# Optimization experiments

Measured on AMD Instinct MI355X. Metric: run time of the kernel, lower is better.

## Reference

```python
import jax, jax.numpy as jnp
import numpy as np

S_LEN = 4096; HID = 2048
NH = 8; NVH = 16; DK = 128; DV = 128
KEY_DIM = NH * DK; VAL_DIM = NVH * DV
CONV = 4; EPS = 1e-6; GVA = NVH // NH
SCALE = DK ** -0.5


def _short_conv_silu(x, w):
    # causal depthwise conv1d + SiLU: x [S, C], w [C, K]
    K = w.shape[1]
    xp = jnp.pad(x, ((K - 1, 0), (0, 0)))
    y = xp[0:S_LEN] * w[:, 0]
    for j in range(1, K):
        y = y + xp[j:j + S_LEN] * w[:, j]
    return jax.nn.silu(y)


def _l2norm(x):
    return x / jnp.sqrt(jnp.sum(x * x, axis=-1, keepdims=True) + EPS)


def _forward(x, Wq, Wk, Wv, Wa, Wb, Wg, Wo, conv_q, conv_k, conv_v, A_log, dt_bias, w_norm):
    q = _short_conv_silu(x @ Wq.T, conv_q)   # [S, KEY_DIM]
    k = _short_conv_silu(x @ Wk.T, conv_k)
    v = _short_conv_silu(x @ Wv.T, conv_v)   # [S, VAL_DIM]
    q = q.reshape(S_LEN, NH, DK)
    k = k.reshape(S_LEN, NH, DK)
    v = v.reshape(S_LEN, NVH, DV)
    # grouped value attention: each k/q head serves GVA value heads
    q = jnp.repeat(q, GVA, axis=1)           # [S, NVH, DK]
    k = jnp.repeat(k, GVA, axis=1)
    q = _l2norm(q) * SCALE
    k = _l2norm(k)
    beta = jax.nn.sigmoid(x @ Wb.T)          # [S, NVH] delta-rule learning rate
    g = -jnp.exp(A_log) * jax.nn.softplus(x @ Wa.T + dt_bias)  # [S, NVH] log-decay <= 0

    def step(S, inp):
        q_t, k_t, v_t, g_t, b_t = inp        # [H,DK],[H,DK],[H,DV],[H],[H]
        S = S * jnp.exp(g_t)[:, None, None]  # gated decay of memory
        pred = jnp.einsum('hk,hkv->hv', k_t, S)
        delta = (v_t - pred) * b_t[:, None]  # delta-rule update direction
        S = S + jnp.einsum('hk,hv->hkv', k_t, delta)
        o_t = jnp.einsum('hk,hkv->hv', q_t, S)
        return S, o_t

    S0 = jnp.zeros((NVH, DK, DV), x.dtype)
    _, o = jax.lax.scan(step, S0, (q, k, v, g, beta))  # o [S, NVH, DV]

    # FusedRMSNormGated: gate with silu, then RMS-normalize over head_v_dim
    gate = (x @ Wg.T).reshape(S_LEN, NVH, DV)
    og = o * jax.nn.silu(gate)
    og = og * jax.lax.rsqrt(jnp.mean(og * og, axis=-1, keepdims=True) + EPS) * w_norm
    return og.reshape(S_LEN, VAL_DIM) @ Wo.T  # [S, HID]


def setup_inputs() -> dict:
    key = jax.random.key(0)
    ks = jax.random.split(key, 16)
    def lin(k, out_dim, in_dim):
        return jax.random.normal(k, (out_dim, in_dim), jnp.float32) * (in_dim ** -0.5)
    dt = jnp.exp(jax.random.uniform(ks[12], (NVH,)) * (np.log(0.1) - np.log(0.001)) + np.log(0.001))
    dt = jnp.maximum(dt, 1e-4)
    return {
        "x": jax.random.normal(ks[0], (S_LEN, HID), jnp.float32),
        "Wq": lin(ks[1], KEY_DIM, HID),
        "Wk": lin(ks[2], KEY_DIM, HID),
        "Wv": lin(ks[3], VAL_DIM, HID),
        "Wa": lin(ks[4], NVH, HID),
        "Wb": lin(ks[5], NVH, HID),
        "Wg": lin(ks[6], VAL_DIM, HID),
        "Wo": lin(ks[7], HID, VAL_DIM),
        "conv_q": jax.random.normal(ks[8], (KEY_DIM, CONV), jnp.float32) * 0.2,
        "conv_k": jax.random.normal(ks[9], (KEY_DIM, CONV), jnp.float32) * 0.2,
        "conv_v": jax.random.normal(ks[10], (VAL_DIM, CONV), jnp.float32) * 0.2,
        "A_log": jnp.log(jax.random.uniform(ks[11], (NVH,), minval=1.0, maxval=16.0)),
        "dt_bias": dt + jnp.log(-jnp.expm1(-dt)),
        "w_norm": jnp.ones((DV,), jnp.float32),
    }


def reference(x, Wq, Wk, Wv, Wa, Wb, Wg, Wo, conv_q, conv_k, conv_v, A_log, dt_bias, w_norm):
    return _forward(x, Wq, Wk, Wv, Wa, Wb, Wg, Wo, conv_q, conv_k, conv_v, A_log, dt_bias, w_norm)
```

## Files before the change

### kernel.cpp

```cpp
#include <hip/hip_runtime.h>
#include <hip/hip_bf16.h>
#include <math.h>

#define S_LEN 4096
#define HID   2048
#define NH    8
#define NVH   16
#define DK    128
#define DV    128
#define KEY_DIM  (NH*DK)
#define VAL_DIM  (NVH*DV)
#define SCALE_Q  0.08838834764831845f
#define CCH 64
#define NCH (S_LEN/CCH)

typedef __attribute__((ext_vector_type(8))) short short8;
typedef __attribute__((ext_vector_type(4))) float f32x4;

__global__ __launch_bounds__(256) void cast_f2b(
    const float* __restrict__ in, __hip_bfloat16* __restrict__ out, int n) {
  int i = (blockIdx.x * 256 + threadIdx.x) * 4;
  if (i >= n) return;
  float4 v = *(const float4*)&in[i];
  union { __hip_bfloat16 b[4]; short4 s; } u;
  u.b[0] = __float2bfloat16(v.x); u.b[1] = __float2bfloat16(v.y);
  u.b[2] = __float2bfloat16(v.z); u.b[3] = __float2bfloat16(v.w);
  *(short4*)&out[i] = u.s;
}

__device__ __forceinline__ void lds_load16(const __hip_bfloat16* g,
                                           __hip_bfloat16* l) {
  __builtin_amdgcn_global_load_lds(
      (const __attribute__((address_space(1))) unsigned int*)g,
      (__attribute__((address_space(3))) unsigned int*)l, 16, 0, 0);
}

__global__ __launch_bounds__(256) void gemm_bf16_bt(
    const __hip_bfloat16* __restrict__ A, const __hip_bfloat16* __restrict__ B,
    float* __restrict__ C, int M, int N, int K) {
  __shared__ __hip_bfloat16 sA[128 * 32];
  __shared__ __hip_bfloat16 sB[128 * 32];
  const int t = threadIdx.x;
  const int wave = t >> 6, lane = t & 63;
  const int bm = blockIdx.y, bn = blockIdx.x;
  const int wm = (wave & 1) * 64, wn = (wave >> 1) * 64;

  f32x4 zero = {0.f, 0.f, 0.f, 0.f};
  f32x4 acc[4][4];
  #pragma unroll
  for (int i = 0; i < 4; i++)
    #pragma unroll
    for (int j = 0; j < 4; j++) acc[i][j] = zero;

  const int r0 = t >> 2,        c0 = (t & 3) * 8;
  const int r1 = (256 + t) >> 2, c1 = ((256 + t) & 3) * 8;
  const __hip_bfloat16* gA0 = A + (size_t)(bm * 128 + r0) * K + c0;
  const __hip_bfloat16* gA1 = A + (size_t)(bm * 128 + r1) * K + c1;
  const __hip_bfloat16* gB0 = B + (size_t)(bn * 128 + r0) * K + c0;
  const __hip_bfloat16* gB1 = B + (size_t)(bn * 128 + r1) * K + c1;
  __hip_bfloat16* lA0 = sA + (size_t)(wave * 64) * 8;
  __hip_bfloat16* lA1 = sA + (size_t)(256 + wave * 64) * 8;
  __hip_bfloat16* lB0 = sB + (size_t)(wave * 64) * 8;
  __hip_bfloat16* lB1 = sB + (size_t)(256 + wave * 64) * 8;

  const int fm = lane & 15, fk = (lane >> 4) * 8;

  for (int k0 = 0; k0 < K; k0 += 32) {
    lds_load16(gA0, lA0); lds_load16(gA1, lA1);
    lds_load16(gB0, lB0); lds_load16(gB1, lB1);
    gA0 += 32; gA1 += 32; gB0 += 32; gB1 += 32;
    __syncthreads();
    short8 a[4], b[4];
    #pragma unroll
    for (int i = 0; i < 4; i++)
      a[i] = *(const short8*)&sA[(size_t)(wm + i * 16 + fm) * 32 + fk];
    #pragma unroll
    for (int j = 0; j < 4; j++)
      b[j] = *(const short8*)&sB[(size_t)(wn + j * 16 + fm) * 32 + fk];
    #pragma unroll
    for (int i = 0; i < 4; i++)
      #pragma unroll
      for (int j = 0; j < 4; j++)
        acc[i][j] = __builtin_amdgcn_mfma_f32_16x16x32_bf16(a[i], b[j], acc[i][j], 0, 0, 0);
    __syncthreads();
  }
  #pragma unroll
  for (int i = 0; i < 4; i++) {
    #pragma unroll
    for (int j = 0; j < 4; j++) {
      int col = bn * 128 + wn + j * 16 + (lane & 15);
      int rw0 = bm * 128 + wm + i * 16 + (lane >> 4) * 4;
      #pragma unroll
      for (int r = 0; r < 4; r++)
        C[(size_t)(rw0 + r) * N + col] = acc[i][j][r];
    }
  }
}

__global__ __launch_bounds__(256) void gemm_bt(
    const float* __restrict__ A, const float* __restrict__ B,
    float* __restrict__ C, int M, int N, int K) {
  __shared__ float As[16][68];
  __shared__ float Bs[16][68];
  const int bm = blockIdx.y, bn = blockIdx.x;
  const int t = threadIdx.x;
  const int tx = t & 15, ty = t >> 4;
  const int lrow = t >> 2;
  const int lk0  = (t & 3) * 4;
  const int arow = bm * 64 + lrow;
  const int brow = bn * 64 + lrow;
  const bool bvalid = brow < N;

  float acc[4][4];
  #pragma unroll
  for (int i = 0; i < 4; i++)
    #pragma unroll
    for (int j = 0; j < 4; j++) acc[i][j] = 0.f;

  for (int k0 = 0; k0 < K; k0 += 16) {
    float4 av = *(const float4*)&A[(size_t)arow * K + k0 + lk0];
    float4 bv = bvalid ? *(const float4*)&B[(size_t)brow * K + k0 + lk0]
                       : make_float4(0.f, 0.f, 0.f, 0.f);
    As[lk0+0][lrow] = av.x; As[lk0+1][lrow] = av.y;
    As[lk0+2][lrow] = av.z; As[lk0+3][lrow] = av.w;
    Bs[lk0+0][lrow] = bv.x; Bs[lk0+1][lrow] = bv.y;
    Bs[lk0+2][lrow] = bv.z; Bs[lk0+3][lrow] = bv.w;
    __syncthreads();
    #pragma unroll
    for (int kk = 0; kk < 16; kk++) {
      float4 a = *(const float4*)&As[kk][ty * 4];
      float4 b = *(const float4*)&Bs[kk][tx * 4];
      float ar[4] = {a.x, a.y, a.z, a.w};
      float br[4] = {b.x, b.y, b.z, b.w};
      #pragma unroll
      for (int i = 0; i < 4; i++)
        #pragma unroll
        for (int j = 0; j < 4; j++) acc[i][j] += ar[i] * br[j];
    }
    __syncthreads();
  }
  #pragma unroll
  for (int i = 0; i < 4; i++) {
    int r = bm * 64 + ty * 4 + i;
    #pragma unroll
    for (int j = 0; j < 4; j++) {
      int c = bn * 64 + tx * 4 + j;
      if (c < N) C[(size_t)r * N + c] = acc[i][j];
    }
  }
}

__global__ __launch_bounds__(128) void conv_qk_kernel(
    const float* __restrict__ pre, const float* __restrict__ cw,
    __hip_bfloat16* __restrict__ out, float scale) {
  const int s = blockIdx.x, h = blockIdx.y, t = threadIdx.x;
  const int c = h * 128 + t;
  const float4 w = *(const float4*)&cw[c * 4];
  float y = pre[(size_t)s * KEY_DIM + c] * w.w;
  if (s >= 1) y += pre[(size_t)(s-1) * KEY_DIM + c] * w.z;
  if (s >= 2) y += pre[(size_t)(s-2) * KEY_DIM + c] * w.y;
  if (s >= 3) y += pre[(size_t)(s-3) * KEY_DIM + c] * w.x;
  float v = y / (1.f + expf(-y));
  float ss = v * v;
  #pragma unroll
  for (int off = 1; off < 64; off <<= 1) ss += __shfl_xor(ss, off, 64);
  __shared__ float red[2];
  if ((t & 63) == 0) red[t >> 6] = ss;
  __syncthreads();
  float inv = scale / sqrtf(red[0] + red[1] + 1e-6f);
  out[((size_t)s * NH + h) * 128 + t] = __float2bfloat16(v * inv);
}

__global__ __launch_bounds__(256) void conv_v_kernel(
    const float* __restrict__ pre, const float* __restrict__ cw,
    float* __restrict__ out) {
  const int id = blockIdx.x * 256 + threadIdx.x;
  const int s = id >> 11, c = id & 2047;
  const float4 w = *(const float4*)&cw[c * 4];
  float y = pre[id] * w.w;
  if (s >= 1) y += pre[id - VAL_DIM]     * w.z;
  if (s >= 2) y += pre[id - 2*VAL_DIM]   * w.y;
  if (s >= 3) y += pre[id - 3*VAL_DIM]   * w.x;
  out[id] = y / (1.f + expf(-y));
}

__global__ __launch_bounds__(256) void gb_kernel(
    const float* __restrict__ a_pre, const float* __restrict__ b_pre,
    const float* __restrict__ A_log, const float* __restrict__ dt_bias,
    float* __restrict__ gl, float* __restrict__ bv) {
  const int id = blockIdx.x * 256 + threadIdx.x;
  const int h = id & 15;
  float av = a_pre[id] + dt_bias[h];
  float sp = av > 20.f ? av : log1pf(expf(av));
  gl[id] = -expf(A_log[h]) * sp;
  bv[id] = 1.f / (1.f + expf(-b_pre[id]));
}

__global__ __launch_bounds__(256) void phaseA_kernel(
    const __hip_bfloat16* __restrict__ kn, const float* __restrict__ vc,
    const float* __restrict__ gl, const float* __restrict__ bvv,
    __hip_bfloat16* __restrict__ Wb, __hip_bfloat16* __restrict__ UbT,
    float* __restrict__ Gbuf) {
  const int h = blockIdx.x, c = blockIdx.y, sh = h >> 1;
  const int t = threadIdx.x, lane = t & 63, w = t >> 6;
  const int fm = lane & 15, fq = lane >> 4;
  __shared__ __hip_bfloat16 kch[64][136];
  __shared__ float vch[64][132];
  __shared__ float mm[64][65];
  __shared__ float sol[64][257];
  __shared__ float Gs[64], bet[64], lamB[64];

  {
    const int r = t >> 2, c0 = (t & 3) * 32;
    const __hip_bfloat16* krow = kn + (size_t)(c*64 + r)*KEY_DIM + sh*128 + c0;
    const float* vrow = vc + (size_t)(c*64 + r)*VAL_DIM + h*128 + c0;
    #pragma unroll
    for (int i = 0; i < 4; i++)
      *(short8*)&kch[r][c0 + 8*i] = *(const short8*)&krow[8*i];
    #pragma unroll
    for (int i = 0; i < 8; i++)
      *(float4*)&vch[r][c0 + 4*i] = *(const float4*)&vrow[4*i];
  }
  if (t < 64) {
    float g = gl[(size_t)(c*64 + t)*NVH + h];
    #pragma unroll
    for (int off = 1; off < 64; off <<= 1) {
      float p = __shfl_up(g, off, 64);
      if (t >= off) g += p;
    }
    Gs[t] = g;
    float b = bvv[(size_t)(c*64 + t)*NVH + h];
    bet[t] = b;
    lamB[t] = b * expf(g);
    Gbuf[((size_t)c*NVH + h)*64 + t] = g;
  }
  __syncthreads();

  {
    f32x4 pacc[4];
    #pragma unroll
    for (int lt = 0; lt < 4; lt++) pacc[lt] = (f32x4){0.f,0.f,0.f,0.f};
    #pragma unroll
    for (int k4 = 0; k4 < 4; k4++) {
      short8 aK = *(const short8*)&kch[16*w + fm][k4*32 + fq*8];
      #pragma unroll
      for (int lt = 0; lt < 4; lt++) {
        short8 bK = *(const short8*)&kch[16*lt + fm][k4*32 + fq*8];
        pacc[lt] = __builtin_amdgcn_mfma_f32_16x16x32_bf16(aK, bK, pacc[lt], 0, 0, 0);
      }
    }
    #pragma unroll
    for (int lt = 0; lt < 4; lt++)
      #pragma unroll
      for (int r2 = 0; r2 < 4; r2++) {
        const int j = 16*w + fq*4 + r2, l = 16*lt + fm;
        mm[j][l] = (l < j) ? bet[j] * expf(Gs[j] - Gs[l]) * pacc[lt][r2] : 0.f;
      }
  }
  __syncthreads();

  {
    const bool isW = t < 128;
    const int col = t & 127;
    for (int j = 0; j < 64; j++) {
      float s0 = isW ? lamB[j] * __bfloat162float(kch[j][col]) : bet[j] * vch[j][col];
      float s1 = 0.f;
      int l = 0;
      for (; l + 1 < j; l += 2) {
        s0 = fmaf(-mm[j][l],   sol[l][t],   s0);
        s1 = fmaf(-mm[j][l+1], sol[l+1][t], s1);
      }
      if (l < j) s0 = fmaf(-mm[j][l], sol[l][t], s0);
      sol[j][t] = s0 + s1;
    }
  }
  if (t < 128) {
    const size_t base = ((size_t)c*NVH + h) * 64 * 128;
    for (int j = 0; j < 64; j++)
      Wb[base + j*128 + t] = __float2bfloat16(sol[j][t]);
  } else {
    const int n = t - 128;
    const size_t ub = (((size_t)c*NVH + h) * 128 + n) * 64;
    for (int j0 = 0; j0 < 64; j0 += 4) {
      union { unsigned long long u; __hip_bfloat16 b[4]; } p;
      #pragma unroll
      for (int i = 0; i < 4; i++) p.b[i] = __float2bfloat16(sol[j0+i][t]);
      *(unsigned long long*)&UbT[ub + j0] = p.u;
    }
  }
}

__device__ __forceinline__ void bar_lgkm() {
  asm volatile("s_waitcnt lgkmcnt(0)" ::: "memory");
  __builtin_amdgcn_s_barrier();
  asm volatile("" ::: "memory");
}

__global__ __launch_bounds__(512, 2) void phaseB_kernel(
    const __hip_bfloat16* __restrict__ qn, const __hip_bfloat16* __restrict__ kn,
    const __hip_bfloat16* __restrict__ Wb, const __hip_bfloat16* __restrict__ UbT,
    const float* __restrict__ Gbuf,
    __hip_bfloat16* __restrict__ Db, float* __restrict__ obuf) {
  const int bid = blockIdx.x;
  const int h = (bid & 7) | ((bid >> 4) << 3);
  const int vt = (bid >> 3) & 1;
  const int sh = h >> 1;
  const int t = threadIdx.x, lane = t & 63, w = t >> 6;
  const int fm = lane & 15, fq = lane >> 4;
  const int jt = w >> 1;
  const int nh = w & 1;
  const int dt = w >> 1;

  __shared__ __hip_bfloat16 S16T[64][136];
  __shared__ __hip_bfloat16 kT[2][128][72];
  __shared__ __hip_bfloat16 dT[64][72];
  __shared__ float Gs[64];

  const int kj = (t & 15) * 4, kd = (t >> 4) * 4;
  const int j0 = 16*jt + fq*4;

  f32x4 Sacc[2][2];
  #pragma unroll
  for (int ti = 0; ti < 2; ti++)
    #pragma unroll
    for (int i = 0; i < 2; i++) Sacc[ti][i] = (f32x4){0.f,0.f,0.f,0.f};
  for (int i = t; i < 64*136/2; i += 512) ((unsigned int*)S16T)[i] = 0;

  ushort4 krg[4];
  short8 Qnext[4], Qcur[4];
  short8 Wnext[4], Wcur[4];
  unsigned long long Unext[2], Ucur[2];
  float gl64;

  auto prefetch = [&](int c) {
    const int cb = (c*NVH + h) * 64;
    const __hip_bfloat16* qbase = qn + (size_t)(c*64 + 16*jt + fm)*KEY_DIM + sh*128 + fq*8;
    #pragma unroll
    for (int k4 = 0; k4 < 4; k4++)
      Qnext[k4] = *(const short8*)&qbase[k4*32];
    #pragma unroll
    for (int jj = 0; jj < 4; jj++)
      krg[jj] = *(const ushort4*)&kn[(size_t)(c*64 + kj + jj)*KEY_DIM + sh*128 + kd];
    #pragma unroll
    for (int k4 = 0; k4 < 4; k4++)
      Wnext[k4] = *(const short8*)&Wb[(size_t)(cb + 16*jt + fm)*128 + k4*32 + fq*8];
    #pragma unroll
    for (int i = 0; i < 2; i++) {
      const int tj = 2*nh + i;
      Unext[i] = *(const unsigned long long*)
          &UbT[(((size_t)c*NVH + h)*128 + vt*64 + 16*tj + fm)*64 + j0];
    }
    if (t < 64) gl64 = Gbuf[(size_t)cb + t];
  };

  auto stage = [&](int buf) {
    if (t < 64) Gs[t] = gl64;
    union { ushort4 v[4]; unsigned short u[16]; } kk;
    #pragma unroll
    for (int jj = 0; jj < 4; jj++) kk.v[jj] = krg[jj];
    #pragma unroll
    for (int dd = 0; dd < 4; dd++) {
      union { unsigned short u[4]; unsigned long long q; } p;
      #pragma unroll
      for (int jj = 0; jj < 4; jj++) p.u[jj] = kk.u[jj*4 + dd];
      *(unsigned long long*)&kT[buf][kd + dd][kj] = p.q;
    }
  };

  prefetch(0);
  #pragma unroll
  for (int k4 = 0; k4 < 4; k4++) { Qcur[k4] = Qnext[k4]; Wcur[k4] = Wnext[k4]; }
  #pragma unroll
  for (int i = 0; i < 2; i++) Ucur[i] = Unext[i];
  bar_lgkm();
  stage(0);
  bar_lgkm();

  for (int c = 0; c < NCH; c++) {
    prefetch(c + 1 < NCH ? c + 1 : 0);

    f32x4 aX[2], aO[2];
    #pragma unroll
    for (int i = 0; i < 2; i++) {
      aX[i] = (f32x4){0.f,0.f,0.f,0.f};
      aO[i] = (f32x4){0.f,0.f,0.f,0.f};
    }
    __builtin_amdgcn_s_setprio(1);
    #pragma unroll
    for (int k4 = 0; k4 < 4; k4++) {
      #pragma unroll
      for (int i = 0; i < 2; i++) {
        const int tj = 2*nh + i;
        short8 b = *(const short8*)&S16T[16*tj + fm][k4*32 + fq*8];
        aX[i] = __builtin_amdgcn_mfma_f32_16x16x32_bf16(Wcur[k4], b, aX[i], 0, 0, 0);
        aO[i] = __builtin_amdgcn_mfma_f32_16x16x32_bf16(Qcur[k4], b, aO[i], 0, 0, 0);
      }
    }
    __builtin_amdgcn_s_setprio(0);
    const int cb = (c*NVH + h) * 64;
    const float gC = Gs[63];
    float er[4], os[4];
    #pragma unroll
    for (int r2 = 0; r2 < 4; r2++) {
      const float gj = Gs[j0 + r2];
      os[r2] = expf(gj);
      er[r2] = expf(gC - gj);
    }
    #pragma unroll
    for (int i = 0; i < 2; i++) {
      const int tj = 2*nh + i;
      const int n = 16*tj + fm;
      union { unsigned long long u; __hip_bfloat16 b[4]; } u4;
      u4.u = Ucur[i];
      union { __hip_bfloat16 b[4]; unsigned long long u; } pd;
      #pragma unroll
      for (int r2 = 0; r2 < 4; r2++) {
        const int j = j0 + r2;
        float d = __bfloat162float(u4.b[r2]) - aX[i][r2];
        Db[(size_t)(cb + j)*128 + vt*64 + n] = __float2bfloat16(d);
        pd.b[r2] = __float2bfloat16(d * er[r2]);
        obuf[((size_t)(c*64 + j)*NVH + h)*128 + vt*64 + n] = aO[i][r2] * os[r2];
      }
      *(unsigned long long*)&dT[n][j0] = pd.u;
    }
    const float lamC = expf(gC);
    #pragma unroll
    for (int ti = 0; ti < 2; ti++)
      #pragma unroll
      for (int i = 0; i < 2; i++)
        #pragma unroll
        for (int r2 = 0; r2 < 4; r2++) Sacc[ti][i][r2] *= lamC;
    bar_lgkm();
    __builtin_amdgcn_s_setprio(1);
    #pragma unroll
    for (int ti = 0; ti < 2; ti++) {
      const int m0 = 32*dt + 16*ti;
      #pragma unroll
      for (int kk0 = 0; kk0 < 64; kk0 += 32) {
        short8 aK = *(const short8*)&kT[c & 1][m0 + fm][kk0 + fq*8];
        #pragma unroll
        for (int i = 0; i < 2; i++) {
          const int tj = 2*nh + i;
          short8 bD = *(const short8*)&dT[16*tj + fm][kk0 + fq*8];
          Sacc[ti][i] = __builtin_amdgcn_mfma_f32_16x16x32_bf16(aK, bD, Sacc[ti][i], 0, 0, 0);
        }
      }
    }
    __builtin_amdgcn_s_setprio(0);
    #pragma unroll
    for (int ti = 0; ti < 2; ti++) {
      const int dk0 = 32*dt + 16*ti + fq*4;
      #pragma unroll
      for (int i = 0; i < 2; i++) {
        const int tj = 2*nh + i;
        const int n = 16*tj + fm;
        union { __hip_bfloat16 b[4]; unsigned long long u; } ps;
        #pragma unroll
        for (int r2 = 0; r2 < 4; r2++) ps.b[r2] = __float2bfloat16(Sacc[ti][i][r2]);
        *(unsigned long long*)&S16T[n][dk0] = ps.u;
      }
    }
    stage((c + 1) & 1);
    #pragma unroll
    for (int k4 = 0; k4 < 4; k4++) { Qcur[k4] = Qnext[k4]; Wcur[k4] = Wnext[k4]; }
    #pragma unroll
    for (int i = 0; i < 2; i++) Ucur[i] = Unext[i];
    bar_lgkm();
  }
}

__global__ __launch_bounds__(256) void phaseC_kernel(
    const __hip_bfloat16* __restrict__ qn, const __hip_bfloat16* __restrict__ kn,
    const float* __restrict__ Gbuf, const __hip_bfloat16* __restrict__ Db,
    float* __restrict__ obuf) {
  const int h = blockIdx.x, c = blockIdx.y, sh = h >> 1;
  const int t = threadIdx.x, lane = t & 63, w = t >> 6;
  const int fm = lane & 15, fq = lane >> 4;
  __shared__ __hip_bfloat16 qch[64][136];
  __shared__ __hip_bfloat16 kch[64][136];
  __shared__ __hip_bfloat16 dchT[128][72];
  __shared__ __hip_bfloat16 Pbf[64][72];
  __shared__ float Gs[64];

  {
    const int r = t >> 2, c0 = (t & 3) * 32;
    const __hip_bfloat16* qrow = qn + (size_t)(c*64 + r)*KEY_DIM + sh*128 + c0;
    const __hip_bfloat16* krow = kn + (size_t)(c*64 + r)*KEY_DIM + sh*128 + c0;
    #pragma unroll
    for (int i = 0; i < 4; i++) {
      *(short8*)&qch[r][c0 + 8*i] = *(const short8*)&qrow[8*i];
      *(short8*)&kch[r][c0 + 8*i] = *(const short8*)&krow[8*i];
    }
    const __hip_bfloat16* drow = Db + ((size_t)c*NVH + h)*64*128 + (size_t)r*128 + c0;
    #pragma unroll
    for (int i = 0; i < 4; i++) {
      union { short8 s; unsigned short u[8]; } dv;
      dv.s = *(const short8*)&drow[8*i];
      #pragma unroll
      for (int e = 0; e < 8; e++)
        *(unsigned short*)&dchT[c0 + 8*i + e][r] = dv.u[e];
    }
  }
  if (t < 64) Gs[t] = Gbuf[((size_t)c*NVH + h)*64 + t];
  __syncthreads();

  {
    f32x4 pacc[4];
    #pragma unroll
    for (int lt = 0; lt < 4; lt++) pacc[lt] = (f32x4){0.f,0.f,0.f,0.f};
    #pragma unroll
    for (int k4 = 0; k4 < 4; k4++) {
      short8 aQ = *(const short8*)&qch[16*w + fm][k4*32 + fq*8];
      #pragma unroll
      for (int lt = 0; lt < 4; lt++) {
        short8 bK = *(const short8*)&kch[16*lt + fm][k4*32 + fq*8];
        pacc[lt] = __builtin_amdgcn_mfma_f32_16x16x32_bf16(aQ, bK, pacc[lt], 0, 0, 0);
      }
    }
    #pragma unroll
    for (int lt = 0; lt < 4; lt++)
      #pragma unroll
      for (int r2 = 0; r2 < 4; r2++) {
        const int j = 16*w + fq*4 + r2, l = 16*lt + fm;
        float v = (l <= j) ? expf(Gs[j] - Gs[l]) * pacc[lt][r2] : 0.f;
        Pbf[j][l] = __float2bfloat16(v);
      }
  }

  {
    f32x4 oacc[8];
    #pragma unroll
    for (int nt = 0; nt < 8; nt++) oacc[nt] = (f32x4){0.f,0.f,0.f,0.f};
    #pragma unroll
    for (int ks = 0; ks < 2; ks++) {
      short8 aP = *(const short8*)&Pbf[16*w + fm][ks*32 + fq*8];
      #pragma unroll
      for (int nt = 0; nt < 8; nt++) {
        short8 bD = *(const short8*)&dchT[16*nt + fm][ks*32 + fq*8];
        oacc[nt] = __builtin_amdgcn_mfma_f32_16x16x32_bf16(aP, bD, oacc[nt], 0, 0, 0);
      }
    }
    #pragma unroll
    for (int nt = 0; nt < 8; nt++)
      #pragma unroll
      for (int r2 = 0; r2 < 4; r2++) {
        const int j = 16*w + fq*4 + r2, n = 16*nt + fm;
        float* p = &obuf[((size_t)(c*64 + j)*NVH + h)*128 + n];
        *p += oacc[nt][r2];
      }
  }
}

__global__ __launch_bounds__(128) void norm_kernel(
    const float* __restrict__ o, const float* __restrict__ gate,
    const float* __restrict__ w_norm, __hip_bfloat16* __restrict__ og) {
  const int s = blockIdx.x, h = blockIdx.y, t = threadIdx.x;
  const size_t idx = (size_t)s * VAL_DIM + h * 128 + t;
  float gt = gate[idx];
  float val = o[idx] * (gt / (1.f + expf(-gt)));
  float ss = val * val;
  #pragma unroll
  for (int off = 1; off < 64; off <<= 1) ss += __shfl_xor(ss, off, 64);
  __shared__ float red[2];
  if ((t & 63) == 0) red[t >> 6] = ss;
  __syncthreads();
  float ms = (red[0] + red[1]) * (1.f / 128.f);
  og[idx] = __float2bfloat16(val * (1.f / sqrtf(ms + 1e-6f)) * w_norm[t]);
}

extern "C" void kernel_launch(void* const* d_in, const int* in_sizes, int n_in,
                              void* d_out, int out_size, void* d_ws, size_t ws_size,
                              hipStream_t stream) {
  const float* x       = (const float*)d_in[0];
  const float* Wq      = (const float*)d_in[1];
  const float* Wk      = (const float*)d_in[2];
  const float* Wv      = (const float*)d_in[3];
  const float* Wa      = (const float*)d_in[4];
  const float* Wb_     = (const float*)d_in[5];
  const float* Wg      = (const float*)d_in[6];
  const float* Wo      = (const float*)d_in[7];
  const float* conv_q  = (const float*)d_in[8];
  const float* conv_k  = (const float*)d_in[9];
  const float* conv_v  = (const float*)d_in[10];
  const float* A_log   = (const float*)d_in[11];
  const float* dt_bias = (const float*)d_in[12];
  const float* w_norm  = (const float*)d_in[13];
  float* out = (float*)d_out;

  const size_t QK = (size_t)S_LEN * KEY_DIM;
  const size_t SV = (size_t)S_LEN * VAL_DIM;
  const size_t SM = (size_t)S_LEN * NVH;

  float* W = (float*)d_ws;
  float* q_pre = W;
  float* k_pre = q_pre + QK;
  float* v_pre = k_pre + QK;
  float* qn    = v_pre + SV;
  float* kn    = qn + QK;
  float* vcb   = kn + QK;
  float* a_pre = vcb + SV;
  float* b_pre = a_pre + SM;
  float* glb   = b_pre + SM;
  float* beta  = glb + SM;
  float* Gbuf  = beta + SM;
  __hip_bfloat16* xb = (__hip_bfloat16*)(Gbuf + SM);
  __hip_bfloat16* wb = xb + SV;

  float* gate = q_pre;
  float* obuf = vcb;
  __hip_bfloat16* qnb = (__hip_bfloat16*)qn;
  __hip_bfloat16* knb = (__hip_bfloat16*)kn;
  __hip_bfloat16* ogb = (__hip_bfloat16*)kn;
  __hip_bfloat16* Wbb = xb;
  __hip_bfloat16* UbT = (__hip_bfloat16*)v_pre;
  __hip_bfloat16* Db  = (__hip_bfloat16*)(v_pre + SV/2);

  const int NC = 256 * 4;
  cast_f2b<<<(S_LEN*HID)/NC, 256, 0, stream>>>(x, xb, S_LEN*HID);

  cast_f2b<<<(KEY_DIM*HID)/NC, 256, 0, stream>>>(Wq, wb, KEY_DIM*HID);
  gemm_bf16_bt<<<dim3(KEY_DIM/128, S_LEN/128), 256, 0, stream>>>(xb, wb, q_pre, S_LEN, KEY_DIM, HID);
  cast_f2b<<<(KEY_DIM*HID)/NC, 256, 0, stream>>>(Wk, wb, KEY_DIM*HID);
  gemm_bf16_bt<<<dim3(KEY_DIM/128, S_LEN/128), 256, 0, stream>>>(xb, wb, k_pre, S_LEN, KEY_DIM, HID);
  cast_f2b<<<(VAL_DIM*HID)/NC, 256, 0, stream>>>(Wv, wb, VAL_DIM*HID);
  gemm_bf16_bt<<<dim3(VAL_DIM/128, S_LEN/128), 256, 0, stream>>>(xb, wb, v_pre, S_LEN, VAL_DIM, HID);
  gemm_bt<<<dim3(1, S_LEN/64), 256, 0, stream>>>(x, Wa, a_pre, S_LEN, NVH, HID);
  gemm_bt<<<dim3(1, S_LEN/64), 256, 0, stream>>>(x, Wb_, b_pre, S_LEN, NVH, HID);

  conv_qk_kernel<<<dim3(S_LEN, NH), 128, 0, stream>>>(q_pre, conv_q, qnb, SCALE_Q);
  conv_qk_kernel<<<dim3(S_LEN, NH), 128, 0, stream>>>(k_pre, conv_k, knb, 1.f);
  conv_v_kernel<<<(S_LEN*VAL_DIM)/256, 256, 0, stream>>>(v_pre, conv_v, vcb);
  gb_kernel<<<(S_LEN*NVH)/256, 256, 0, stream>>>(a_pre, b_pre, A_log, dt_bias, glb, beta);

  cast_f2b<<<(VAL_DIM*HID)/NC, 256, 0, stream>>>(Wg, wb, VAL_DIM*HID);
  gemm_bf16_bt<<<dim3(VAL_DIM/128, S_LEN/128), 256, 0, stream>>>(xb, wb, gate, S_LEN, VAL_DIM, HID);

  phaseA_kernel<<<dim3(NVH, NCH), 256, 0, stream>>>(knb, vcb, glb, beta, Wbb, UbT, Gbuf);
  phaseB_kernel<<<2*NVH, 512, 0, stream>>>(qnb, knb, Wbb, UbT, Gbuf, Db, obuf);
  phaseC_kernel<<<dim3(NVH, NCH), 256, 0, stream>>>(qnb, knb, Gbuf, Db, obuf);

  norm_kernel<<<dim3(S_LEN, NVH), 128, 0, stream>>>(obuf, gate, w_norm, ogb);

  cast_f2b<<<(HID*VAL_DIM)/NC, 256, 0, stream>>>(Wo, wb, HID*VAL_DIM);
  gemm_bf16_bt<<<dim3(HID/128, S_LEN/128), 256, 0, stream>>>(ogb, wb, out, S_LEN, HID, VAL_DIM);
}
```

Measured before the change: 1.201 ms.

## Fuse Q/K/V/gate projections into one GEMM and batch weight casts

```diff
diff --git a/kernel.cpp b/kernel.cpp
--- a/kernel.cpp
+++ b/kernel.cpp
@@ -10,6 +10,7 @@
 #define DV    128
 #define KEY_DIM  (NH*DK)
 #define VAL_DIM  (NVH*DV)
+#define NPROJ 6144
 #define SCALE_Q  0.08838834764831845f
 #define CCH 64
 #define NCH (S_LEN/CCH)
@@ -26,6 +27,24 @@
   u.b[0] = __float2bfloat16(v.x); u.b[1] = __float2bfloat16(v.y);
   u.b[2] = __float2bfloat16(v.z); u.b[3] = __float2bfloat16(v.w);
   *(short4*)&out[i] = u.s;
+}
+
+__global__ __launch_bounds__(256) void cast5(
+    const float* __restrict__ w0, const float* __restrict__ w1,
+    const float* __restrict__ w2, const float* __restrict__ w3,
+    const float* __restrict__ w4, __hip_bfloat16* __restrict__ dst) {
+  int i = (blockIdx.x * 256 + threadIdx.x) * 4;
+  const float* src; int off;
+  if      (i <  2097152) { src = w0; off = 0; }
+  else if (i <  4194304) { src = w1; off = 2097152; }
+  else if (i <  8388608) { src = w2; off = 4194304; }
+  else if (i < 12582912) { src = w3; off = 8388608; }
+  else                   { src = w4; off = 12582912; }
+  float4 v = *(const float4*)&src[i - off];
+  union { __hip_bfloat16 b[4]; short4 s; } u;
+  u.b[0] = __float2bfloat16(v.x); u.b[1] = __float2bfloat16(v.y);
+  u.b[2] = __float2bfloat16(v.z); u.b[3] = __float2bfloat16(v.w);
+  *(short4*)&dst[i] = u.s;
 }
 
 __device__ __forceinline__ void lds_load16(const __hip_bfloat16* g,
@@ -97,19 +116,22 @@
   }
 }
 
-__global__ __launch_bounds__(256) void gemm_bt(
-    const float* __restrict__ A, const float* __restrict__ B,
-    float* __restrict__ C, int M, int N, int K) {
+__global__ __launch_bounds__(256) void gemm_bt2(
+    const float* __restrict__ A, const float* __restrict__ Ba,
+    const float* __restrict__ Bb, float* __restrict__ Ca,
+    float* __restrict__ Cb, int K) {
+  const float* B = blockIdx.x == 0 ? Ba : Bb;
+  float* C       = blockIdx.x == 0 ? Ca : Cb;
+  const int N = NVH;
   __shared__ float As[16][68];
   __shared__ float Bs[16][68];
-  const int bm = blockIdx.y, bn = blockIdx.x;
+  const int bm = blockIdx.y;
   const int t = threadIdx.x;
   const int tx = t & 15, ty = t >> 4;
   const int lrow = t >> 2;
   const int lk0  = (t & 3) * 4;
   const int arow = bm * 64 + lrow;
-  const int brow = bn * 64 + lrow;
-  const bool bvalid = brow < N;
+  const bool bvalid = lrow < N;
 
   float acc[4][4];
   #pragma unroll
@@ -119,7 +141,7 @@
 
   for (int k0 = 0; k0 < K; k0 += 16) {
     float4 av = *(const float4*)&A[(size_t)arow * K + k0 + lk0];
-    float4 bv = bvalid ? *(const float4*)&B[(size_t)brow * K + k0 + lk0]
+    float4 bv = bvalid ? *(const float4*)&B[(size_t)lrow * K + k0 + lk0]
                        : make_float4(0.f, 0.f, 0.f, 0.f);
     As[lk0+0][lrow] = av.x; As[lk0+1][lrow] = av.y;
     As[lk0+2][lrow] = av.z; As[lk0+3][lrow] = av.w;
@@ -144,30 +166,38 @@
     int r = bm * 64 + ty * 4 + i;
     #pragma unroll
     for (int j = 0; j < 4; j++) {
-      int c = bn * 64 + tx * 4 + j;
+      int c = tx * 4 + j;
       if (c < N) C[(size_t)r * N + c] = acc[i][j];
     }
   }
 }
 
 __global__ __launch_bounds__(128) void conv_qk_kernel(
-    const float* __restrict__ pre, const float* __restrict__ cw,
-    __hip_bfloat16* __restrict__ out, float scale) {
-  const int s = blockIdx.x, h = blockIdx.y, t = threadIdx.x;
-  const int c = h * 128 + t;
-  const float4 w = *(const float4*)&cw[c * 4];
-  float y = pre[(size_t)s * KEY_DIM + c] * w.w;
-  if (s >= 1) y += pre[(size_t)(s-1) * KEY_DIM + c] * w.z;
-  if (s >= 2) y += pre[(size_t)(s-2) * KEY_DIM + c] * w.y;
-  if (s >= 3) y += pre[(size_t)(s-3) * KEY_DIM + c] * w.x;
-  float v = y / (1.f + expf(-y));
+    const float* __restrict__ pre, const float* __restrict__ cwq,
+    const float* __restrict__ cwk, __hip_bfloat16* __restrict__ qn,
+    __hip_bfloat16* __restrict__ kn) {
+  const int s = blockIdx.x, y = blockIdx.y, t = threadIdx.x;
+  const bool isq = y < 8;
+  const int h = isq ? y : y - 8;
+  const int ch = h * 128 + t;
+  const float* cw = isq ? cwq : cwk;
+  const int col = (isq ? 0 : 1024) + ch;
+  const float4 w = *(const float4*)&cw[ch * 4];
+  const size_t base = (size_t)s * NPROJ + col;
+  float v0 = pre[base] * w.w;
+  if (s >= 1) v0 += pre[base - NPROJ]     * w.z;
+  if (s >= 2) v0 += pre[base - 2*NPROJ]   * w.y;
+  if (s >= 3) v0 += pre[base - 3*NPROJ]   * w.x;
+  float v = v0 / (1.f + expf(-v0));
   float ss = v * v;
   #pragma unroll
   for (int off = 1; off < 64; off <<= 1) ss += __shfl_xor(ss, off, 64);
   __shared__ float red[2];
   if ((t & 63) == 0) red[t >> 6] = ss;
   __syncthreads();
+  const float scale = isq ? SCALE_Q : 1.f;
   float inv = scale / sqrtf(red[0] + red[1] + 1e-6f);
+  __hip_bfloat16* out = isq ? qn : kn;
   out[((size_t)s * NH + h) * 128 + t] = __float2bfloat16(v * inv);
 }
 
@@ -177,10 +207,11 @@
   const int id = blockIdx.x * 256 + threadIdx.x;
   const int s = id >> 11, c = id & 2047;
   const float4 w = *(const float4*)&cw[c * 4];
-  float y = pre[id] * w.w;
-  if (s >= 1) y += pre[id - VAL_DIM]     * w.z;
-  if (s >= 2) y += pre[id - 2*VAL_DIM]   * w.y;
-  if (s >= 3) y += pre[id - 3*VAL_DIM]   * w.x;
+  const size_t base = (size_t)s * NPROJ + 2048 + c;
+  float y = pre[base] * w.w;
+  if (s >= 1) y += pre[base - NPROJ]     * w.z;
+  if (s >= 2) y += pre[base - 2*NPROJ]   * w.y;
+  if (s >= 3) y += pre[base - 3*NPROJ]   * w.x;
   out[id] = y / (1.f + expf(-y));
 }
 
@@ -552,11 +583,12 @@
 }
 
 __global__ __launch_bounds__(128) void norm_kernel(
-    const float* __restrict__ o, const float* __restrict__ gate,
+    const float* __restrict__ o, const float* __restrict__ pre,
     const float* __restrict__ w_norm, __hip_bfloat16* __restrict__ og) {
   const int s = blockIdx.x, h = blockIdx.y, t = threadIdx.x;
   const size_t idx = (size_t)s * VAL_DIM + h * 128 + t;
-  float gt = gate[idx];
+  const size_t gidx = (size_t)s * NPROJ + 4096 + h * 128 + t;
+  float gt = pre[gidx];
   float val = o[idx] * (gt / (1.f + expf(-gt)));
   float ss = val * val;
   #pragma unroll
@@ -587,60 +619,35 @@
   const float* w_norm  = (const float*)d_in[13];
   float* out = (float*)d_out;
 
-  const size_t QK = (size_t)S_LEN * KEY_DIM;
-  const size_t SV = (size_t)S_LEN * VAL_DIM;
-  const size_t SM = (size_t)S_LEN * NVH;
-
   float* W = (float*)d_ws;
-  float* q_pre = W;
-  float* k_pre = q_pre + QK;
-  float* v_pre = k_pre + QK;
-  float* qn    = v_pre + SV;
-  float* kn    = qn + QK;
-  float* vcb   = kn + QK;
-  float* a_pre = vcb + SV;
-  float* b_pre = a_pre + SM;
-  float* glb   = b_pre + SM;
-  float* beta  = glb + SM;
-  float* Gbuf  = beta + SM;
-  __hip_bfloat16* xb = (__hip_bfloat16*)(Gbuf + SM);
-  __hip_bfloat16* wb = xb + SV;
-
-  float* gate = q_pre;
+  float* pre   = W;
+  __hip_bfloat16* qn = (__hip_bfloat16*)(W + 25165824);
+  __hip_bfloat16* kn = (__hip_bfloat16*)(W + 27262976);
+  float* vcb   = W + 29360128;
+  float* a_pre = W + 37748736;
+  float* b_pre = a_pre + 65536;
+  float* glb   = b_pre + 65536;
+  float* beta  = glb + 65536;
+  float* Gbuf  = beta + 65536;
+  __hip_bfloat16* xb  = (__hip_bfloat16*)(W + 38076416);
+  __hip_bfloat16* wts = xb + 8388608;
+  __hip_bfloat16* wo  = wts + 12582912;
+  __hip_bfloat16* Wbb = (__hip_bfloat16*)(W + 50659328);
+  __hip_bfloat16* UbT = (__hip_bfloat16*)(W + 38076416);
+  __hip_bfloat16* Db  = (__hip_bfloat16*)(W + 38076416 + 4194304);
+  __hip_bfloat16* ogb = Db;
   float* obuf = vcb;
-  __hip_bfloat16* qnb = (__hip_bfloat16*)qn;
-  __hip_bfloat16* knb = (__hip_bfloat16*)kn;
-  __hip_bfloat16* ogb = (__hip_bfloat16*)kn;
-  __hip_bfloat16* Wbb = xb;
-  __hip_bfloat16* UbT = (__hip_bfloat16*)v_pre;
-  __hip_bfloat16* Db  = (__hip_bfloat16*)(v_pre + SV/2);
-
-  const int NC = 256 * 4;
-  cast_f2b<<<(S_LEN*HID)/NC, 256, 0, stream>>>(x, xb, S_LEN*HID);
-
-  cast_f2b<<<(KEY_DIM*HID)/NC, 256, 0, stream>>>(Wq, wb, KEY_DIM*HID);
-  gemm_bf16_bt<<<dim3(KEY_DIM/128, S_LEN/128), 256, 0, stream>>>(xb, wb, q_pre, S_LEN, KEY_DIM, HID);
-  cast_f2b<<<(KEY_DIM*HID)/NC, 256, 0, stream>>>(Wk, wb, KEY_DIM*HID);
-  gemm_bf16_bt<<<dim3(KEY_DIM/128, S_LEN/128), 256, 0, stream>>>(xb, wb, k_pre, S_LEN, KEY_DIM, HID);
-  cast_f2b<<<(VAL_DIM*HID)/NC, 256, 0, stream>>>(Wv, wb, VAL_DIM*HID);
-  gemm_bf16_bt<<<dim3(VAL_DIM/128, S_LEN/128), 256, 0, stream>>>(xb, wb, v_pre, S_LEN, VAL_DIM, HID);
-  gemm_bt<<<dim3(1, S_LEN/64), 256, 0, stream>>>(x, Wa, a_pre, S_LEN, NVH, HID);
-  gemm_bt<<<dim3(1, S_LEN/64), 256, 0, stream>>>(x, Wb_, b_pre, S_LEN, NVH, HID);
-
-  conv_qk_kernel<<<dim3(S_LEN, NH), 128, 0, stream>>>(q_pre, conv_q, qnb, SCALE_Q);
-  conv_qk_kernel<<<dim3(S_LEN, NH), 128, 0, stream>>>(k_pre, conv_k, knb, 1.f);
-  conv_v_kernel<<<(S_LEN*VAL_DIM)/256, 256, 0, stream>>>(v_pre, conv_v, vcb);
+
+  cast_f2b<<<(S_LEN*HID)/1024, 256, 0, stream>>>(x, xb, S_LEN*HID);
+  cast5<<<16777216/1024, 256, 0, stream>>>(Wq, Wk, Wv, Wg, Wo, wts);
+  gemm_bt2<<<dim3(2, S_LEN/64), 256, 0, stream>>>(x, Wa, Wb_, a_pre, b_pre, HID);
+  gemm_bf16_bt<<<dim3(NPROJ/128, S_LEN/128), 256, 0, stream>>>(xb, wts, pre, S_LEN, NPROJ, HID);
+  conv_qk_kernel<<<dim3(S_LEN, 16), 128, 0, stream>>>(pre, conv_q, conv_k, qn, kn);
+  conv_v_kernel<<<(S_LEN*VAL_DIM)/256, 256, 0, stream>>>(pre, conv_v, vcb);
   gb_kernel<<<(S_LEN*NVH)/256, 256, 0, stream>>>(a_pre, b_pre, A_log, dt_bias, glb, beta);
-
-  cast_f2b<<<(VAL_DIM*HID)/NC, 256, 0, stream>>>(Wg, wb, VAL_DIM*HID);
-  gemm_bf16_bt<<<dim3(VAL_DIM/128, S_LEN/128), 256, 0, stream>>>(xb, wb, gate, S_LEN, VAL_DIM, HID);
-
-  phaseA_kernel<<<dim3(NVH, NCH), 256, 0, stream>>>(knb, vcb, glb, beta, Wbb, UbT, Gbuf);
-  phaseB_kernel<<<2*NVH, 512, 0, stream>>>(qnb, knb, Wbb, UbT, Gbuf, Db, obuf);
-  phaseC_kernel<<<dim3(NVH, NCH), 256, 0, stream>>>(qnb, knb, Gbuf, Db, obuf);
-
-  norm_kernel<<<dim3(S_LEN, NVH), 128, 0, stream>>>(obuf, gate, w_norm, ogb);
-
-  cast_f2b<<<(HID*VAL_DIM)/NC, 256, 0, stream>>>(Wo, wb, HID*VAL_DIM);
-  gemm_bf16_bt<<<dim3(HID/128, S_LEN/128), 256, 0, stream>>>(ogb, wb, out, S_LEN, HID, VAL_DIM);
-}
+  phaseA_kernel<<<dim3(NVH, NCH), 256, 0, stream>>>(kn, vcb, glb, beta, Wbb, UbT, Gbuf);
+  phaseB_kernel<<<2*NVH, 512, 0, stream>>>(qn, kn, Wbb, UbT, Gbuf, Db, obuf);
+  phaseC_kernel<<<dim3(NVH, NCH), 256, 0, stream>>>(qn, kn, Gbuf, Db, obuf);
+  norm_kernel<<<dim3(S_LEN, NVH), 128, 0, stream>>>(obuf, pre, w_norm, ogb);
+  gemm_bf16_bt<<<dim3(HID/128, S_LEN/128), 256, 0, stream>>>(ogb, wo, out, S_LEN, HID, VAL_DIM);
+}
```

Result: faster. 1.000 ms (-16.7%).
